# Kernel optimization log

Hardware: AMD Instinct MI355X
Metric: run time of the kernel (lower is better)

## Reference

```python
import jax, jax.numpy as jnp
import numpy as np

SMOOTH = 1e-5
ALPHA = 0.25
GAMMA = 2.0
INIT_BETA = 0.5
BETA_DECAY = 0.99


def setup_inputs() -> dict:
    key = jax.random.key(0)
    ks = jax.random.split(key, 7)
    B, NC, C, H, W, D = 8, 1000, 19, 512, 512, 768
    return {
        "logits": jax.random.normal(ks[0], (B, NC), dtype=jnp.float32),
        "label": jax.random.randint(ks[1], (B,), 0, NC),
        "vision_feat": jax.random.normal(ks[2], (B, D), dtype=jnp.float32),
        "text_feat": jax.random.normal(ks[3], (B, D), dtype=jnp.float32),
        "modal_mask": jax.random.uniform(ks[4], (B, 2), dtype=jnp.float32),
        "seg_mask": jax.random.normal(ks[5], (B, C, H, W), dtype=jnp.float32),
        "seg_gt": jax.random.randint(ks[6], (B, H, W), 0, C),
        "epoch": 5,
    }


def _ce_mean(logits, label):
    logp = jax.nn.log_softmax(logits, axis=-1)
    return -jnp.take_along_axis(logp, label[:, None], axis=-1).mean()


def _dice_loss(pred, target):
    # pred: [B,C,H,W] (raw, as in the torch module), target: [B,H,W] int
    C = pred.shape[1]
    onehot = (target[:, None, :, :] == jnp.arange(C)[None, :, None, None]).astype(pred.dtype)
    inter = jnp.sum(pred * onehot, axis=(2, 3))          # [B,C]
    union = jnp.sum(pred, axis=(2, 3)) + jnp.sum(onehot, axis=(2, 3))
    dice = (2.0 * inter + SMOOTH) / (union + SMOOTH)
    return jnp.mean(1.0 - dice)


def _focal_loss(pred, target):
    # pred: [B,C,H,W] logits over class axis 1
    logp = jax.nn.log_softmax(pred, axis=1)
    logp_t = jnp.take_along_axis(logp, target[:, None, :, :], axis=1)[:, 0]  # [B,H,W]
    p_t = jnp.exp(logp_t)
    ce = -logp_t
    return jnp.mean(ALPHA * (1.0 - p_t) ** GAMMA * ce)


def _modal_balance(vision_feat, text_feat, modal_mask, epoch):
    beta_t = INIT_BETA * BETA_DECAY ** epoch
    vn = vision_feat / jnp.linalg.norm(vision_feat, axis=1, keepdims=True)
    tn = text_feat / jnp.linalg.norm(text_feat, axis=1, keepdims=True)
    v_cons = jnp.mean((vn - vn.mean(axis=0, keepdims=True)) ** 2)
    t_cons = jnp.mean((tn - tn.mean(axis=0, keepdims=True)) ** 2)
    cross = 1.0 - jnp.mean(jnp.sum(vn * tn, axis=1))  # cosine sim of unit vectors
    return ((1.0 - beta_t) * v_cons * modal_mask[:, 0].mean()
            + beta_t * t_cons * modal_mask[:, 1].mean() + cross)


def reference(logits, label, vision_feat, text_feat, modal_mask, seg_mask, seg_gt, epoch):
    ce = _ce_mean(logits, label)
    mb = _modal_balance(vision_feat, text_feat, modal_mask, epoch)
    seg = _dice_loss(seg_mask, seg_gt) + _focal_loss(seg_mask, seg_gt)
    total = ce + 0.3 * mb + 0.5 * seg
    return total
```

## Files before the change

### kernel.cpp

```cpp
#include <hip/hip_runtime.h>
#include <math.h>

#define SMOOTH_F 1e-5f
#define ALPHA_F 0.25f

constexpr int Bn = 8;
constexpr int NCn = 1000;
constexpr int Cn = 19;
constexpr int HWn = 512 * 512;
constexpr int Dn = 768;
constexpr int BC = Bn * Cn;

constexpr int TPB = 256;
constexpr int NCHUNK = 4;
constexpr int G4 = HWn / 4;
constexpr int GRPS_PER_BLK = TPB * NCHUNK;
constexpr int BLKS_PER_B = G4 / GRPS_PER_BLK;
constexpr int SEG_BLOCKS = Bn * BLKS_PER_B;

constexpr int PLANE = SEG_BLOCKS;
constexpr int NPLANES = 3 * Cn + 1;

__device__ __forceinline__ float wave_sum(float v) {
#pragma unroll
  for (int off = 32; off > 0; off >>= 1) v += __shfl_down(v, off, 64);
  return v;
}
__device__ __forceinline__ float wave_max(float v) {
#pragma unroll
  for (int off = 32; off > 0; off >>= 1) v = fmaxf(v, __shfl_down(v, off, 64));
  return v;
}

__global__ __launch_bounds__(TPB, 2) void k_seg(
    const float* __restrict__ pred, const int* __restrict__ gt,
    float* __restrict__ ws) {
  __shared__ float s_inter[Cn];
  __shared__ float s_count[Cn];
  __shared__ float s_pred[Cn];
  __shared__ float s_red[4];

  const int tid = threadIdx.x;
  const int wid = tid >> 6, lane = tid & 63;
  const int sblk = blockIdx.x;
  const int b = sblk >> 6;
  const unsigned gbase4 = (unsigned)(sblk & 63) * GRPS_PER_BLK;

  const float* pbase = pred + (size_t)b * Cn * HWn;
  const int* gtb = gt + (size_t)b * HWn;

  if (tid < Cn) { s_inter[tid] = 0.0f; s_count[tid] = 0.0f; s_pred[tid] = 0.0f; }
  __syncthreads();

  float psum[Cn];
#pragma unroll
  for (int c = 0; c < Cn; ++c) psum[c] = 0.0f;
  float focal = 0.0f;

  float4 xA[Cn], xB[Cn];
  int4 tA, tB;

  auto issue = [&](float4 (&x)[Cn], int4& t4, int k) {
    const unsigned goff = (gbase4 + (unsigned)k * TPB + (unsigned)tid) << 4;
    asm volatile("global_load_dwordx4 %0, %1, %2"
                 : "=v"(t4) : "v"(goff), "s"(gtb));
#pragma unroll
    for (int c = 0; c < Cn; ++c) {
      const unsigned off = goff + ((unsigned)c << 20);
      asm volatile("global_load_dwordx4 %0, %1, %2"
                   : "=v"(x[c]) : "v"(off), "s"(pbase));
    }
  };

  auto compute = [&](const float4 (&x)[Cn], const int4& t4) {
    float4 se = make_float4(0.0f, 0.0f, 0.0f, 0.0f);
    float4 xt = make_float4(0.0f, 0.0f, 0.0f, 0.0f);
#pragma unroll
    for (int c = 0; c < Cn; ++c) {
      const float4 v = x[c];
      psum[c] += v.x + v.y + v.z + v.w;
      se.x += __expf(v.x);
      se.y += __expf(v.y);
      se.z += __expf(v.z);
      se.w += __expf(v.w);
      if (t4.x == c) xt.x = v.x;
      if (t4.y == c) xt.y = v.y;
      if (t4.z == c) xt.z = v.z;
      if (t4.w == c) xt.w = v.w;
    }
#pragma unroll
    for (int j = 0; j < 4; ++j) {
      const float sej = (j == 0) ? se.x : (j == 1) ? se.y : (j == 2) ? se.z : se.w;
      const float xtj = (j == 0) ? xt.x : (j == 1) ? xt.y : (j == 2) ? xt.z : xt.w;
      const int t     = (j == 0) ? t4.x : (j == 1) ? t4.y : (j == 2) ? t4.z : t4.w;
      const float lpt = xtj - __logf(sej);
      const float p = __expf(lpt);
      const float om = 1.0f - p;
      focal += om * om * (-lpt);
      atomicAdd(&s_inter[t], xtj);
      atomicAdd(&s_count[t], 1.0f);
    }
  };

  issue(xA, tA, 0);
  issue(xB, tB, 1);

  asm volatile("s_waitcnt vmcnt(20)");
  __builtin_amdgcn_sched_barrier(0);
  compute(xA, tA);
  issue(xA, tA, 2);

  asm volatile("s_waitcnt vmcnt(20)");
  __builtin_amdgcn_sched_barrier(0);
  compute(xB, tB);
  issue(xB, tB, 3);

  asm volatile("s_waitcnt vmcnt(20)");
  __builtin_amdgcn_sched_barrier(0);
  compute(xA, tA);

  asm volatile("s_waitcnt vmcnt(0)");
  __builtin_amdgcn_sched_barrier(0);
  compute(xB, tB);

#pragma unroll
  for (int c = 0; c < Cn; ++c) {
    float pc = wave_sum(psum[c]);
    if (lane == 0) atomicAdd(&s_pred[c], pc);
  }
  const float fw = wave_sum(focal * ALPHA_F);
  if (lane == 0) s_red[wid] = fw;
  __syncthreads();

  if (tid < Cn) {
    ws[(size_t)tid * PLANE + sblk] = s_inter[tid];
    ws[(size_t)(Cn + tid) * PLANE + sblk] = s_pred[tid];
    ws[(size_t)(2 * Cn + tid) * PLANE + sblk] = s_count[tid];
  }
  if (tid == 0)
    ws[(size_t)(3 * Cn) * PLANE + sblk] = s_red[0] + s_red[1] + s_red[2] + s_red[3];
}

__global__ __launch_bounds__(1024) void k_final(
    const float* __restrict__ ws, const float* __restrict__ logits,
    const int* __restrict__ label, const float* __restrict__ vf,
    const float* __restrict__ tf, const float* __restrict__ mmask,
    const int* __restrict__ epoch, float* __restrict__ out) {
  __shared__ float s_sum[3 * BC];
  __shared__ float s_d[3];
  __shared__ float s_f, s_ce, s_mb;
  const int tid = threadIdx.x;
  const int wid = tid >> 6, lane = tid & 63;

  if (tid < 3 * BC) {
    const int quant = tid / BC;
    const int pair = tid - quant * BC;
    const int b = pair / Cn;
    const int c = pair - b * Cn;
    const float4* p = (const float4*)(ws + (size_t)(quant * Cn + c) * PLANE +
                                      b * BLKS_PER_B);
    float s = 0.0f;
#pragma unroll
    for (int k = 0; k < 16; ++k) {
      const float4 v = p[k];
      s += v.x + v.y + v.z + v.w;
    }
    s_sum[tid] = s;
  }
  if (wid == 15) {
    const float4* p = (const float4*)(ws + (size_t)(3 * Cn) * PLANE) + lane * 2;
    const float4 v0 = p[0], v1 = p[1];
    float f = v0.x + v0.y + v0.z + v0.w + v1.x + v1.y + v1.z + v1.w;
    f = wave_sum(f);
    if (lane == 0) s_f = f;
  }
  if (wid == 8) {
    float acc = 0.0f;
    for (int b = 0; b < Bn; ++b) {
      const float* row = logits + b * NCn;
      float rv[16];
      float lm = -INFINITY;
#pragma unroll
      for (int k = 0; k < 16; ++k) {
        const int j = lane + 64 * k;
        rv[k] = (j < NCn) ? row[j] : -INFINITY;
        lm = fmaxf(lm, rv[k]);
      }
      lm = wave_max(lm);
      lm = __shfl(lm, 0, 64);
      float ls = 0.0f;
#pragma unroll
      for (int k = 0; k < 16; ++k)
        if (lane + 64 * k < NCn) ls += expf(rv[k] - lm);
      ls = wave_sum(ls);
      if (lane == 0) acc += row[label[b]] - (lm + logf(ls));
    }
    if (lane == 0) s_ce = -(acc / (float)Bn);
  }
  if (wid == 9) {
    float nvv[Bn], ntt[Bn];
    for (int b = 0; b < Bn; ++b) {
      float sv = 0.0f, st = 0.0f;
#pragma unroll
      for (int k = 0; k < 12; ++k) {
        const int j = lane + 64 * k;
        const float a = vf[b * Dn + j];
        const float c = tf[b * Dn + j];
        sv += a * a;
        st += c * c;
      }
      sv = wave_sum(sv);
      st = wave_sum(st);
      nvv[b] = sqrtf(__shfl(sv, 0, 64));
      ntt[b] = sqrtf(__shfl(st, 0, 64));
    }
    float colv = 0.0f, colt = 0.0f, cross = 0.0f;
#pragma unroll 2
    for (int k = 0; k < 12; ++k) {
      const int j = lane + 64 * k;
      float sv = 0.0f, ssv = 0.0f, stt = 0.0f, sst = 0.0f, cr = 0.0f;
#pragma unroll
      for (int b = 0; b < Bn; ++b) {
        const float vn = vf[b * Dn + j] / nvv[b];
        const float tn = tf[b * Dn + j] / ntt[b];
        sv += vn; ssv += vn * vn;
        stt += tn; sst += tn * tn;
        cr += vn * tn;
      }
      colv += ssv - sv * sv * 0.125f;
      colt += sst - stt * stt * 0.125f;
      cross += cr;
    }
    colv = wave_sum(colv);
    colt = wave_sum(colt);
    cross = wave_sum(cross);
    if (lane == 0) {
      const float v_cons = colv / (float)(Bn * Dn);
      const float t_cons = colt / (float)(Bn * Dn);
      const float crossv = 1.0f - cross * 0.125f;
      const float beta = 0.5f * powf(0.99f, (float)epoch[0]);
      float mm0 = 0.0f, mm1 = 0.0f;
      for (int b = 0; b < Bn; ++b) { mm0 += mmask[b * 2]; mm1 += mmask[b * 2 + 1]; }
      mm0 *= 0.125f; mm1 *= 0.125f;
      s_mb = (1.0f - beta) * v_cons * mm0 + beta * t_cons * mm1 + crossv;
    }
  }
  __syncthreads();

  float v = 0.0f;
  if (tid < BC) {
    const float inter = s_sum[0 * BC + tid];
    const float ps    = s_sum[1 * BC + tid];
    const float cnt   = s_sum[2 * BC + tid];
    const float dice = (2.0f * inter + SMOOTH_F) / (ps + cnt + SMOOTH_F);
    v = 1.0f - dice;
  }
  v = wave_sum(v);
  if (lane == 0 && wid < 3) s_d[wid] = v;
  __syncthreads();

  if (tid == 0) {
    const float dice_mean = (s_d[0] + s_d[1] + s_d[2]) / (float)BC;
    const float focal_mean = s_f / (float)(Bn * HWn);
    const float seg = dice_mean + focal_mean;
    out[0] = s_ce + 0.3f * s_mb + 0.5f * seg;
  }
}

extern "C" void kernel_launch(void* const* d_in, const int* in_sizes, int n_in,
                              void* d_out, int out_size, void* d_ws, size_t ws_size,
                              hipStream_t stream) {
  const float* logits = (const float*)d_in[0];
  const int* label    = (const int*)d_in[1];
  const float* vf     = (const float*)d_in[2];
  const float* tf     = (const float*)d_in[3];
  const float* mmask  = (const float*)d_in[4];
  const float* seg    = (const float*)d_in[5];
  const int* gt       = (const int*)d_in[6];
  const int* epoch    = (const int*)d_in[7];
  float* out = (float*)d_out;
  float* ws = (float*)d_ws;

  hipLaunchKernelGGL(k_seg, dim3(SEG_BLOCKS), dim3(TPB), 0, stream, seg, gt, ws);
  hipLaunchKernelGGL(k_final, dim3(1), dim3(1024), 0, stream,
                     ws, logits, label, vf, tf, mmask, epoch, out);
}
```

Measured before the change: 291.9 us.

## Pipeline seg loads per class with triple-buffered channel registers

The load schedule is restructured. Before, each thread loaded all 19 class channels for one pixel group at a time, double-buffered across four chunks. Now each thread owns four pixel groups per wave and streams the class channels one at a time through three rotating register buffers, with fine-grained waitcnt. This cuts the live register footprint from 38 float4 arrays to about 12, which may improve occupancy, and it keeps more loads in flight. It also changes the access pattern to per-class sweeps, which could affect cache and DRAM locality.

```diff
diff --git a/kernel.cpp b/kernel.cpp
--- a/kernel.cpp
+++ b/kernel.cpp
@@ -12,10 +12,7 @@
 constexpr int BC = Bn * Cn;
 
 constexpr int TPB = 256;
-constexpr int NCHUNK = 4;
-constexpr int G4 = HWn / 4;
-constexpr int GRPS_PER_BLK = TPB * NCHUNK;
-constexpr int BLKS_PER_B = G4 / GRPS_PER_BLK;
+constexpr int BLKS_PER_B = 64;
 constexpr int SEG_BLOCKS = Bn * BLKS_PER_B;
 
 constexpr int PLANE = SEG_BLOCKS;
@@ -31,6 +28,31 @@
   for (int off = 32; off > 0; off >>= 1) v = fmaxf(v, __shfl_down(v, off, 64));
   return v;
 }
+
+#define ISSUE(c, X) { \
+  const unsigned voff_ = pxoff + (unsigned)((c) * 0x100000); \
+  asm volatile("global_load_dwordx4 %0, %1, %2"             : "=v"(X[0]) : "v"(voff_), "s"(pbase)); \
+  asm volatile("global_load_dwordx4 %0, %1, %2 offset:1024" : "=v"(X[1]) : "v"(voff_), "s"(pbase)); \
+  asm volatile("global_load_dwordx4 %0, %1, %2 offset:2048" : "=v"(X[2]) : "v"(voff_), "s"(pbase)); \
+  asm volatile("global_load_dwordx4 %0, %1, %2 offset:3072" : "=v"(X[3]) : "v"(voff_), "s"(pbase)); }
+
+#define WAITC(n) { asm volatile("s_waitcnt vmcnt(" #n ")"); \
+                   __builtin_amdgcn_sched_barrier(0); }
+
+#define CONSUME(c, X) { \
+  float pa_ = 0.0f; \
+  _Pragma("unroll") \
+  for (int k = 0; k < 4; ++k) { \
+    const float4 v_ = X[k]; \
+    pa_ += v_.x + v_.y + v_.z + v_.w; \
+    se[k].x += __expf(v_.x); se[k].y += __expf(v_.y); \
+    se[k].z += __expf(v_.z); se[k].w += __expf(v_.w); \
+    if (t4[k].x == (c)) xt[k].x = v_.x; \
+    if (t4[k].y == (c)) xt[k].y = v_.y; \
+    if (t4[k].z == (c)) xt[k].z = v_.z; \
+    if (t4[k].w == (c)) xt[k].w = v_.w; \
+  } \
+  psum[c] = pa_; }
 
 __global__ __launch_bounds__(TPB, 2) void k_seg(
     const float* __restrict__ pred, const int* __restrict__ gt,
@@ -44,84 +66,65 @@
   const int wid = tid >> 6, lane = tid & 63;
   const int sblk = blockIdx.x;
   const int b = sblk >> 6;
-  const unsigned gbase4 = (unsigned)(sblk & 63) * GRPS_PER_BLK;
 
   const float* pbase = pred + (size_t)b * Cn * HWn;
   const int* gtb = gt + (size_t)b * HWn;
+  const unsigned pxoff =
+      ((unsigned)((sblk & 63) * 1024 + wid * 256 + lane)) << 4;
 
   if (tid < Cn) { s_inter[tid] = 0.0f; s_count[tid] = 0.0f; s_pred[tid] = 0.0f; }
   __syncthreads();
 
+  float4 X0[4], X1[4], X2[4];
+  int4 t4[4];
+  float4 se[4], xt[4];
   float psum[Cn];
 #pragma unroll
-  for (int c = 0; c < Cn; ++c) psum[c] = 0.0f;
+  for (int k = 0; k < 4; ++k) {
+    se[k] = make_float4(0.0f, 0.0f, 0.0f, 0.0f);
+    xt[k] = make_float4(0.0f, 0.0f, 0.0f, 0.0f);
+  }
+
+  asm volatile("global_load_dwordx4 %0, %1, %2"             : "=v"(t4[0]) : "v"(pxoff), "s"(gtb));
+  asm volatile("global_load_dwordx4 %0, %1, %2 offset:1024" : "=v"(t4[1]) : "v"(pxoff), "s"(gtb));
+  asm volatile("global_load_dwordx4 %0, %1, %2 offset:2048" : "=v"(t4[2]) : "v"(pxoff), "s"(gtb));
+  asm volatile("global_load_dwordx4 %0, %1, %2 offset:3072" : "=v"(t4[3]) : "v"(pxoff), "s"(gtb));
+
+  ISSUE(0, X0) ISSUE(1, X1) ISSUE(2, X2)
+
+  WAITC(8)  CONSUME(0,  X0) ISSUE(3,  X0)
+  WAITC(8)  CONSUME(1,  X1) ISSUE(4,  X1)
+  WAITC(8)  CONSUME(2,  X2) ISSUE(5,  X2)
+  WAITC(8)  CONSUME(3,  X0) ISSUE(6,  X0)
+  WAITC(8)  CONSUME(4,  X1) ISSUE(7,  X1)
+  WAITC(8)  CONSUME(5,  X2) ISSUE(8,  X2)
+  WAITC(8)  CONSUME(6,  X0) ISSUE(9,  X0)
+  WAITC(8)  CONSUME(7,  X1) ISSUE(10, X1)
+  WAITC(8)  CONSUME(8,  X2) ISSUE(11, X2)
+  WAITC(8)  CONSUME(9,  X0) ISSUE(12, X0)
+  WAITC(8)  CONSUME(10, X1) ISSUE(13, X1)
+  WAITC(8)  CONSUME(11, X2) ISSUE(14, X2)
+  WAITC(8)  CONSUME(12, X0) ISSUE(15, X0)
+  WAITC(8)  CONSUME(13, X1) ISSUE(16, X1)
+  WAITC(8)  CONSUME(14, X2) ISSUE(17, X2)
+  WAITC(8)  CONSUME(15, X0) ISSUE(18, X0)
+  WAITC(8)  CONSUME(16, X1)
+  WAITC(4)  CONSUME(17, X2)
+  WAITC(0)  CONSUME(18, X0)
+
   float focal = 0.0f;
-
-  float4 xA[Cn], xB[Cn];
-  int4 tA, tB;
-
-  auto issue = [&](float4 (&x)[Cn], int4& t4, int k) {
-    const unsigned goff = (gbase4 + (unsigned)k * TPB + (unsigned)tid) << 4;
-    asm volatile("global_load_dwordx4 %0, %1, %2"
-                 : "=v"(t4) : "v"(goff), "s"(gtb));
-#pragma unroll
-    for (int c = 0; c < Cn; ++c) {
-      const unsigned off = goff + ((unsigned)c << 20);
-      asm volatile("global_load_dwordx4 %0, %1, %2"
-                   : "=v"(x[c]) : "v"(off), "s"(pbase));
-    }
-  };
-
-  auto compute = [&](const float4 (&x)[Cn], const int4& t4) {
-    float4 se = make_float4(0.0f, 0.0f, 0.0f, 0.0f);
-    float4 xt = make_float4(0.0f, 0.0f, 0.0f, 0.0f);
-#pragma unroll
-    for (int c = 0; c < Cn; ++c) {
-      const float4 v = x[c];
-      psum[c] += v.x + v.y + v.z + v.w;
-      se.x += __expf(v.x);
-      se.y += __expf(v.y);
-      se.z += __expf(v.z);
-      se.w += __expf(v.w);
-      if (t4.x == c) xt.x = v.x;
-      if (t4.y == c) xt.y = v.y;
-      if (t4.z == c) xt.z = v.z;
-      if (t4.w == c) xt.w = v.w;
-    }
-#pragma unroll
-    for (int j = 0; j < 4; ++j) {
-      const float sej = (j == 0) ? se.x : (j == 1) ? se.y : (j == 2) ? se.z : se.w;
-      const float xtj = (j == 0) ? xt.x : (j == 1) ? xt.y : (j == 2) ? xt.z : xt.w;
-      const int t     = (j == 0) ? t4.x : (j == 1) ? t4.y : (j == 2) ? t4.z : t4.w;
-      const float lpt = xtj - __logf(sej);
-      const float p = __expf(lpt);
-      const float om = 1.0f - p;
-      focal += om * om * (-lpt);
-      atomicAdd(&s_inter[t], xtj);
-      atomicAdd(&s_count[t], 1.0f);
-    }
-  };
-
-  issue(xA, tA, 0);
-  issue(xB, tB, 1);
-
-  asm volatile("s_waitcnt vmcnt(20)");
-  __builtin_amdgcn_sched_barrier(0);
-  compute(xA, tA);
-  issue(xA, tA, 2);
-
-  asm volatile("s_waitcnt vmcnt(20)");
-  __builtin_amdgcn_sched_barrier(0);
-  compute(xB, tB);
-  issue(xB, tB, 3);
-
-  asm volatile("s_waitcnt vmcnt(20)");
-  __builtin_amdgcn_sched_barrier(0);
-  compute(xA, tA);
-
-  asm volatile("s_waitcnt vmcnt(0)");
-  __builtin_amdgcn_sched_barrier(0);
-  compute(xB, tB);
+#pragma unroll
+  for (int k = 0; k < 4; ++k) {
+#define FOCAL1(comp) { \
+    const float lpt_ = xt[k].comp - __logf(se[k].comp); \
+    const float p_ = __expf(lpt_); \
+    const float om_ = 1.0f - p_; \
+    focal += om_ * om_ * (-lpt_); \
+    atomicAdd(&s_inter[t4[k].comp], xt[k].comp); \
+    atomicAdd(&s_count[t4[k].comp], 1.0f); }
+    FOCAL1(x) FOCAL1(y) FOCAL1(z) FOCAL1(w)
+#undef FOCAL1
+  }
 
 #pragma unroll
   for (int c = 0; c < Cn; ++c) {
```

Result: slower. 302.5 us (+3.6%).
